# Kernel optimization log

Hardware: AMD Instinct MI355X
Metric: run time of the kernel (lower is better)

Reference implementation:

```python
import jax, jax.numpy as jnp
import numpy as np

IMAGE = 800.0
HIGH_THRESH = 0.7   # torchvision RPN fg_iou_thresh
LOW_THRESH = 0.3    # torchvision RPN bg_iou_thresh
BELOW_LOW = -1      # Matcher.BELOW_LOW_THRESHOLD
BETWEEN = -2        # Matcher.BETWEEN_THRESHOLDS


def _make_boxes(key, shape, max_wh):
    # shape = (..., 4) target; build valid xyxy boxes inside the image
    k1, k2 = jax.random.split(key)
    xy = jax.random.uniform(k1, shape[:-1] + (2,)) * (IMAGE - max_wh)
    wh = jax.random.uniform(k2, shape[:-1] + (2,)) * (max_wh - 4.0) + 4.0
    return jnp.concatenate([xy, xy + wh], axis=-1)


def setup_inputs() -> dict:
    key = jax.random.key(0)
    kA, kG, kS, kC = jax.random.split(key, 4)
    B, A, G = 4, 160000, 64
    anchors = _make_boxes(kA, (B, A, 4), 128.0)
    gt_boxes = _make_boxes(kG, (B, G, 4), 200.0)
    # soft score labels in {0, 0.5, 1} style: mostly 1, some <1 (ignored), some 0
    u = jax.random.uniform(kS, (B, G))
    score_labels = jnp.where(u < 0.15, 0.0, jnp.where(u < 0.3, 0.5, 1.0)).astype(jnp.float32)
    confidence_labels = jax.random.randint(kC, (B, G), 0, 2).astype(jnp.int32)
    return {"anchors": anchors, "gt_boxes": gt_boxes,
            "score_labels": score_labels, "confidence_labels": confidence_labels}


def _box_iou(a, b):
    # a: [G,4] gt, b: [A,4] anchors -> [G,A]
    area_a = (a[:, 2] - a[:, 0]) * (a[:, 3] - a[:, 1])          # [G]
    area_b = (b[:, 2] - b[:, 0]) * (b[:, 3] - b[:, 1])          # [A]
    lt = jnp.maximum(a[:, None, :2], b[None, :, :2])            # [G,A,2]
    rb = jnp.minimum(a[:, None, 2:], b[None, :, 2:])            # [G,A,2]
    wh = jnp.clip(rb - lt, 0.0)
    inter = wh[..., 0] * wh[..., 1]                              # [G,A]
    return inter / (area_a[:, None] + area_b[None, :] - inter)


def _matcher(mq):
    # torchvision Matcher with allow_low_quality_matches=True. mq: [G,A]
    matched_vals = mq.max(axis=0)                                # [A]
    matches = mq.argmax(axis=0).astype(jnp.int32)                # [A]
    m = jnp.where(matched_vals < LOW_THRESH, BELOW_LOW,
                  jnp.where(matched_vals < HIGH_THRESH, BETWEEN, matches))
    # restore, for each gt, anchors achieving that gt's max IoU
    highest_per_gt = mq.max(axis=1, keepdims=True)               # [G,1]
    low_quality = (mq == highest_per_gt).any(axis=0)             # [A]
    return jnp.where(low_quality, matches, m)


def _assign_one(anchors, gt, scores, confs):
    mq = _box_iou(gt, anchors)                                   # [G,A]
    midx = _matcher(mq)                                          # [A]
    cl = jnp.clip(midx, 0)
    matched_gt = gt[cl]                                          # [A,4]
    pos = midx >= 0
    labels = pos.astype(jnp.float32)
    labels = jnp.minimum(labels, scores[cl])
    labels = jnp.where(midx == BELOW_LOW, 0.0, labels)
    labels = jnp.where(midx == BETWEEN, -1.0, labels)
    labels = jnp.where((scores[cl] < 1.0) & pos, -1.0, labels)
    labels = jnp.where((confs[cl] == 0) & pos, -1.0, labels)
    return labels, matched_gt


def reference(anchors, gt_boxes, score_labels, confidence_labels):
    labels, matched_gt_boxes = jax.vmap(_assign_one)(anchors, gt_boxes, score_labels, confidence_labels)
    return labels, matched_gt_boxes
```

## Files before the change

kernel.cpp:

```cpp
#include <hip/hip_runtime.h>

constexpr int NB = 4;
constexpr int NA = 160000;
constexpr int NG = 64;

constexpr int P1   = 250;
constexpr int APB1 = NA / P1;
constexpr int APW  = 40;
constexpr int AB2  = 512;
constexpr int GX2  = (NA + AB2 - 1) / AB2;

__device__ __forceinline__ float box_area(float x0, float y0, float x1, float y1) {
#pragma clang fp contract(off)
    return (x1 - x0) * (y1 - y0);
}

__device__ __forceinline__ void inter_denom(float gx0, float gy0, float gx1, float gy1, float garea,
                                            float ax0, float ay0, float ax1, float ay1, float aarea,
                                            float& inter, float& denom) {
#pragma clang fp contract(off)
    float ltx = fmaxf(gx0, ax0);
    float lty = fmaxf(gy0, ay0);
    float rbx = fminf(gx1, ax1);
    float rby = fminf(gy1, ay1);
    float w = fmaxf(rbx - ltx, 0.0f);
    float h = fmaxf(rby - lty, 0.0f);
    inter = w * h;
    float s = garea + aarea;
    denom = s - inter;
}

__device__ __forceinline__ bool frac_gt(float i1, float d1, float i2, float d2) {
#pragma clang fp contract(off)
    float p1 = i1 * d2;
    float p2 = i2 * d1;
    float e1 = fmaf(i1, d2, -p1);
    float e2 = fmaf(i2, d1, -p2);
    return (p1 > p2) || ((p1 == p2) && (e1 > e2));
}

__device__ __forceinline__ float div_rn(float n, float d) {
    float y = __builtin_amdgcn_rcpf(d);
    float e = fmaf(-d, y, 1.0f);
    y = fmaf(e, y, y);
    float q = n * y;
    float r = fmaf(-d, q, n);
    q = fmaf(r, y, q);
    float r2 = fmaf(-d, q, n);
    return fmaf(r2, y, q);
}

__global__ __launch_bounds__(1024, 2) void k_part(
        const float* __restrict__ anchors, const float* __restrict__ gts,
        float2* __restrict__ part ) {
    __shared__ float4 sa[APB1];
    __shared__ float pi[16][NG], pd[16][NG];

    const int b = blockIdx.y;
    const int j = blockIdx.x;
    const int lane = threadIdx.x & 63;
    const int wid = __builtin_amdgcn_readfirstlane(threadIdx.x >> 6);

    const float4* __restrict__ anc =
        reinterpret_cast<const float4*>(anchors) + (size_t)b * NA;
    if (threadIdx.x < APB1)
        sa[threadIdx.x] = anc[j * APB1 + threadIdx.x];

    float4 g = reinterpret_cast<const float4*>(gts)[b * NG + lane];
    float garea = box_area(g.x, g.y, g.z, g.w);
    __syncthreads();

    float bi = 0.0f, bd = 1.0f;
#pragma unroll 8
    for (int i = 0; i < APW; ++i) {
        float4 a = sa[wid * APW + i];
        float aarea = box_area(a.x, a.y, a.z, a.w);
        float inter, denom;
        inter_denom(g.x, g.y, g.z, g.w, garea, a.x, a.y, a.z, a.w, aarea,
                    inter, denom);
        if (frac_gt(inter, denom, bi, bd)) { bi = inter; bd = denom; }
    }

    pi[wid][lane] = bi;
    pd[wid][lane] = bd;
    __syncthreads();
    if (threadIdx.x < NG) {
        float ci = pi[0][threadIdx.x], cd = pd[0][threadIdx.x];
#pragma unroll
        for (int wv = 1; wv < 16; ++wv) {
            float ni = pi[wv][threadIdx.x], nd = pd[wv][threadIdx.x];
            if (frac_gt(ni, nd, ci, cd)) { ci = ni; cd = nd; }
        }
        part[((size_t)b * P1 + j) * NG + threadIdx.x] = make_float2(ci, cd);
    }
}

__global__ __launch_bounds__(256, 2) void k_assign2(
        const float* __restrict__ anchors, const float* __restrict__ gts,
        const float* __restrict__ scores, const int* __restrict__ confs,
        const float2* __restrict__ part,
        float* __restrict__ labels_out, float4* __restrict__ boxes_out) {
    __shared__ float4 sg[NG];
    __shared__ float2 sah[NG];
    __shared__ float  ssc[NG];
    __shared__ int    scf[NG];
    __shared__ float  rpi[4][NG], rpd[4][NG];

    const int b = blockIdx.y;
    if (threadIdx.x < NG) {
        const int gi = threadIdx.x;
        sg[gi]  = reinterpret_cast<const float4*>(gts)[b * NG + gi];
        ssc[gi] = scores[b * NG + gi];
        scf[gi] = confs[b * NG + gi];
    }

    {
        const int gi = threadIdx.x & 63;
        const int c  = threadIdx.x >> 6;
        float ci = 0.0f, cd = 1.0f;
#pragma unroll 8
        for (int p = c; p < P1; p += 4) {
            float2 v = part[((size_t)b * P1 + p) * NG + gi];
            if (frac_gt(v.x, v.y, ci, cd)) { ci = v.x; cd = v.y; }
        }
        rpi[c][gi] = ci;
        rpd[c][gi] = cd;
    }
    __syncthreads();
    if (threadIdx.x < NG) {
        const int gi = threadIdx.x;
        float ci = rpi[0][gi], cd = rpd[0][gi];
#pragma unroll
        for (int wv = 1; wv < 4; ++wv) {
            float ni = rpi[wv][gi], nd = rpd[wv][gi];
            if (frac_gt(ni, nd, ci, cd)) { ci = ni; cd = nd; }
        }
        float4 gv = sg[gi];
        sah[gi] = make_float2(box_area(gv.x, gv.y, gv.z, gv.w),
                              div_rn(ci, cd));
    }
    __syncthreads();

    const int base2 = blockIdx.x * AB2;
    const float4* __restrict__ anc =
        reinterpret_cast<const float4*>(anchors) + (size_t)b * NA;

    float4 av[2];
    float  aarea[2];
    float  best[2]    = {-1.0f, -1.0f};
    int    matches[2] = {0, 0};
    bool   lowq[2]    = {false, false};
#pragma unroll
    for (int k = 0; k < 2; ++k) {
        int ai = base2 + threadIdx.x + k * 256;
        int ac = ai < NA ? ai : NA - 1;
        av[k] = anc[ac];
        aarea[k] = box_area(av[k].x, av[k].y, av[k].z, av[k].w);
    }

#pragma unroll 4
    for (int g = 0; g < NG; ++g) {
        float4 gb = sg[g];
        float2 ah = sah[g];
#pragma unroll
        for (int k = 0; k < 2; ++k) {
            float inter, denom;
            inter_denom(gb.x, gb.y, gb.z, gb.w, ah.x,
                        av[k].x, av[k].y, av[k].z, av[k].w, aarea[k],
                        inter, denom);
            float v = div_rn(inter, denom);
            if (v > best[k]) { best[k] = v; matches[k] = g; }
            lowq[k] |= (v == ah.y);
        }
    }

#pragma unroll
    for (int k = 0; k < 2; ++k) {
        int ai = base2 + threadIdx.x + k * 256;
        if (ai >= NA) continue;

        int m    = (best[k] < 0.3f) ? -1 : ((best[k] < 0.7f) ? -2 : matches[k]);
        int midx = lowq[k] ? matches[k] : m;
        int cl   = (midx < 0) ? 0 : midx;

        float4 mg = sg[cl];
        float  sc = ssc[cl];
        int    cf = scf[cl];

        bool pos = (midx >= 0);
        float lab = pos ? 1.0f : 0.0f;
        lab = fminf(lab, sc);
        if (midx == -1) lab = 0.0f;
        if (midx == -2) lab = -1.0f;
        if (sc < 1.0f && pos) lab = -1.0f;
        if (cf == 0 && pos) lab = -1.0f;

        labels_out[(size_t)b * NA + ai] = lab;
        boxes_out[(size_t)b * NA + ai] = mg;
    }
}

__global__ __launch_bounds__(256) void k_gt_highest_fb(
        const float* __restrict__ anchors, const float* __restrict__ gts,
        float* __restrict__ highest ) {
    const int b = blockIdx.y;
    const int lane = threadIdx.x & 63;
    const int wid = __builtin_amdgcn_readfirstlane(threadIdx.x >> 6);

    const float4* __restrict__ anc =
        reinterpret_cast<const float4*>(anchors) + (size_t)b * NA;
    float4 g = reinterpret_cast<const float4*>(gts)[b * NG + lane];
    float garea = box_area(g.x, g.y, g.z, g.w);

    const int base = blockIdx.x * 160 + wid * 40;
    float bi = 0.0f, bd = 1.0f;
#pragma unroll 8
    for (int i = 0; i < 40; ++i) {
        float4 a = anc[base + i];
        float aarea = box_area(a.x, a.y, a.z, a.w);
        float inter, denom;
        inter_denom(g.x, g.y, g.z, g.w, garea, a.x, a.y, a.z, a.w, aarea,
                    inter, denom);
        if (frac_gt(inter, denom, bi, bd)) { bi = inter; bd = denom; }
    }

    __shared__ float pi[4][NG], pd[4][NG];
    pi[wid][lane] = bi;
    pd[wid][lane] = bd;
    __syncthreads();
    if (threadIdx.x < NG) {
        float ci = pi[0][threadIdx.x], cd = pd[0][threadIdx.x];
#pragma unroll
        for (int wv = 1; wv < 4; ++wv) {
            float ni = pi[wv][threadIdx.x], nd = pd[wv][threadIdx.x];
            if (frac_gt(ni, nd, ci, cd)) { ci = ni; cd = nd; }
        }
        atomicMax(reinterpret_cast<int*>(&highest[b * NG + threadIdx.x]),
                  __float_as_int(div_rn(ci, cd)));
    }
}

__global__ __launch_bounds__(256) void k_assign_fb(
        const float* __restrict__ anchors, const float* __restrict__ gts,
        const float* __restrict__ scores, const int* __restrict__ confs,
        const float* __restrict__ highest,
        float* __restrict__ labels_out, float4* __restrict__ boxes_out) {
    __shared__ float4 sg[NG];
    __shared__ float2 sah[NG];
    __shared__ float  ssc[NG];
    __shared__ int    scf[NG];

    const int b = blockIdx.y;
    if (threadIdx.x < NG) {
        const int gi = threadIdx.x;
        float4 gv = reinterpret_cast<const float4*>(gts)[b * NG + gi];
        sg[gi] = gv;
        sah[gi] = make_float2(box_area(gv.x, gv.y, gv.z, gv.w),
                              highest[b * NG + gi]);
        ssc[gi] = scores[b * NG + gi];
        scf[gi] = confs[b * NG + gi];
    }
    __syncthreads();

    const int ai = blockIdx.x * 256 + threadIdx.x;
    const float4* __restrict__ anc =
        reinterpret_cast<const float4*>(anchors) + (size_t)b * NA;
    float4 av = anc[ai];
    float aarea = box_area(av.x, av.y, av.z, av.w);

    float best = -1.0f;
    int   matches = 0;
    bool  lowq = false;
#pragma unroll 4
    for (int g = 0; g < NG; ++g) {
        float4 gb = sg[g];
        float2 ah = sah[g];
        float inter, denom;
        inter_denom(gb.x, gb.y, gb.z, gb.w, ah.x,
                    av.x, av.y, av.z, av.w, aarea, inter, denom);
        float v = div_rn(inter, denom);
        if (v > best) { best = v; matches = g; }
        lowq |= (v == ah.y);
    }

    int m    = (best < 0.3f) ? -1 : ((best < 0.7f) ? -2 : matches);
    int midx = lowq ? matches : m;
    int cl   = (midx < 0) ? 0 : midx;

    float4 mg = sg[cl];
    float  sc = ssc[cl];
    int    cf = scf[cl];

    bool pos = (midx >= 0);
    float lab = pos ? 1.0f : 0.0f;
    lab = fminf(lab, sc);
    if (midx == -1) lab = 0.0f;
    if (midx == -2) lab = -1.0f;
    if (sc < 1.0f && pos) lab = -1.0f;
    if (cf == 0 && pos) lab = -1.0f;

    labels_out[(size_t)b * NA + ai] = lab;
    boxes_out[(size_t)b * NA + ai] = mg;
}

extern "C" void kernel_launch(void* const* d_in, const int* in_sizes, int n_in,
                              void* d_out, int out_size, void* d_ws, size_t ws_size,
                              hipStream_t stream) {
    const float* anchors = (const float*)d_in[0];
    const float* gts     = (const float*)d_in[1];
    const float* scores  = (const float*)d_in[2];
    const int*   confs   = (const int*)d_in[3];

    float* labels_out = (float*)d_out;
    float4* boxes_out = (float4*)((float*)d_out + (size_t)NB * NA);

    const size_t need = (size_t)NB * P1 * NG * sizeof(float2);
    if (ws_size >= need) {
        float2* part = (float2*)d_ws;
        dim3 g1(P1, NB), g2(GX2, NB);
        k_part<<<g1, dim3(1024), 0, stream>>>(anchors, gts, part);
        k_assign2<<<g2, dim3(256), 0, stream>>>(anchors, gts, scores, confs,
                                                part, labels_out, boxes_out);
    } else {
        float* highest = (float*)d_ws;
        hipMemsetAsync(d_ws, 0, (size_t)NB * NG * sizeof(float), stream);
        dim3 g1(1000, NB), g2(625, NB), blk(256);
        k_gt_highest_fb<<<g1, blk, 0, stream>>>(anchors, gts, highest);
        k_assign_fb<<<g2, blk, 0, stream>>>(anchors, gts, scores, confs,
                                            highest, labels_out, boxes_out);
    }
}
```

Measured before the change: 137.4 us.

## Fold partial-max reduction into k_part via last-block atomic counter

The first kernel now reduces its per-block partial maxima in the last-arriving block per batch, using a global atomic counter and agent-scope atomic loads and stores. It writes the final per-gt highest IoU directly. The assign kernel now reads precomputed highest values instead of re-reducing 250 partials in every block, and it processes one anchor per thread with a 625-block grid and higher occupancy launch bounds. This removes redundant per-block reduction work, at the cost of a serialized tail reduction and a counter that relies on modulo wraparound across calls.

```diff
diff --git a/kernel.cpp b/kernel.cpp
--- a/kernel.cpp
+++ b/kernel.cpp
@@ -7,8 +7,8 @@
 constexpr int P1   = 250;
 constexpr int APB1 = NA / P1;
 constexpr int APW  = 40;
-constexpr int AB2  = 512;
-constexpr int GX2  = (NA + AB2 - 1) / AB2;
+
+__device__ int g_ctr[NB];
 
 __device__ __forceinline__ float box_area(float x0, float y0, float x1, float y1) {
 #pragma clang fp contract(off)
@@ -50,11 +50,22 @@
     return fmaf(r2, y, q);
 }
 
-__global__ __launch_bounds__(1024, 2) void k_part(
+__device__ __forceinline__ unsigned long long pack2(float x, float y) {
+    return (unsigned long long)__float_as_uint(x) |
+           ((unsigned long long)__float_as_uint(y) << 32);
+}
+__device__ __forceinline__ void unpack2(unsigned long long u, float& x, float& y) {
+    x = __uint_as_float((unsigned)(u & 0xffffffffu));
+    y = __uint_as_float((unsigned)(u >> 32));
+}
+
+__global__ __launch_bounds__(1024, 8) void k_part(
         const float* __restrict__ anchors, const float* __restrict__ gts,
-        float2* __restrict__ part ) {
+        float2* __restrict__ part ,
+        float* __restrict__ highest ) {
     __shared__ float4 sa[APB1];
     __shared__ float pi[16][NG], pd[16][NG];
+    __shared__ int s_old;
 
     const int b = blockIdx.y;
     const int j = blockIdx.x;
@@ -71,7 +82,7 @@
     __syncthreads();
 
     float bi = 0.0f, bd = 1.0f;
-#pragma unroll 8
+#pragma unroll 4
     for (int i = 0; i < APW; ++i) {
         float4 a = sa[wid * APW + i];
         float aarea = box_area(a.x, a.y, a.z, a.w);
@@ -91,156 +102,49 @@
             float ni = pi[wv][threadIdx.x], nd = pd[wv][threadIdx.x];
             if (frac_gt(ni, nd, ci, cd)) { ci = ni; cd = nd; }
         }
-        part[((size_t)b * P1 + j) * NG + threadIdx.x] = make_float2(ci, cd);
-    }
-}
-
-__global__ __launch_bounds__(256, 2) void k_assign2(
-        const float* __restrict__ anchors, const float* __restrict__ gts,
-        const float* __restrict__ scores, const int* __restrict__ confs,
-        const float2* __restrict__ part,
-        float* __restrict__ labels_out, float4* __restrict__ boxes_out) {
-    __shared__ float4 sg[NG];
-    __shared__ float2 sah[NG];
-    __shared__ float  ssc[NG];
-    __shared__ int    scf[NG];
-    __shared__ float  rpi[4][NG], rpd[4][NG];
-
-    const int b = blockIdx.y;
-    if (threadIdx.x < NG) {
-        const int gi = threadIdx.x;
-        sg[gi]  = reinterpret_cast<const float4*>(gts)[b * NG + gi];
-        ssc[gi] = scores[b * NG + gi];
-        scf[gi] = confs[b * NG + gi];
-    }
+        __hip_atomic_store(
+            reinterpret_cast<unsigned long long*>(
+                &part[((size_t)b * P1 + j) * NG + threadIdx.x]),
+            pack2(ci, cd), __ATOMIC_RELAXED, __HIP_MEMORY_SCOPE_AGENT);
+    }
+    __syncthreads();
+    if (threadIdx.x == 0) {
+        __threadfence();
+        s_old = atomicAdd(&g_ctr[b], 1);
+    }
+    __syncthreads();
+    if ((s_old % P1) != P1 - 1) return;
 
     {
         const int gi = threadIdx.x & 63;
         const int c  = threadIdx.x >> 6;
         float ci = 0.0f, cd = 1.0f;
-#pragma unroll 8
-        for (int p = c; p < P1; p += 4) {
-            float2 v = part[((size_t)b * P1 + p) * NG + gi];
-            if (frac_gt(v.x, v.y, ci, cd)) { ci = v.x; cd = v.y; }
-        }
-        rpi[c][gi] = ci;
-        rpd[c][gi] = cd;
-    }
-    __syncthreads();
-    if (threadIdx.x < NG) {
-        const int gi = threadIdx.x;
-        float ci = rpi[0][gi], cd = rpd[0][gi];
-#pragma unroll
-        for (int wv = 1; wv < 4; ++wv) {
-            float ni = rpi[wv][gi], nd = rpd[wv][gi];
-            if (frac_gt(ni, nd, ci, cd)) { ci = ni; cd = nd; }
-        }
-        float4 gv = sg[gi];
-        sah[gi] = make_float2(box_area(gv.x, gv.y, gv.z, gv.w),
-                              div_rn(ci, cd));
-    }
-    __syncthreads();
-
-    const int base2 = blockIdx.x * AB2;
-    const float4* __restrict__ anc =
-        reinterpret_cast<const float4*>(anchors) + (size_t)b * NA;
-
-    float4 av[2];
-    float  aarea[2];
-    float  best[2]    = {-1.0f, -1.0f};
-    int    matches[2] = {0, 0};
-    bool   lowq[2]    = {false, false};
-#pragma unroll
-    for (int k = 0; k < 2; ++k) {
-        int ai = base2 + threadIdx.x + k * 256;
-        int ac = ai < NA ? ai : NA - 1;
-        av[k] = anc[ac];
-        aarea[k] = box_area(av[k].x, av[k].y, av[k].z, av[k].w);
-    }
-
 #pragma unroll 4
-    for (int g = 0; g < NG; ++g) {
-        float4 gb = sg[g];
-        float2 ah = sah[g];
-#pragma unroll
-        for (int k = 0; k < 2; ++k) {
-            float inter, denom;
-            inter_denom(gb.x, gb.y, gb.z, gb.w, ah.x,
-                        av[k].x, av[k].y, av[k].z, av[k].w, aarea[k],
-                        inter, denom);
-            float v = div_rn(inter, denom);
-            if (v > best[k]) { best[k] = v; matches[k] = g; }
-            lowq[k] |= (v == ah.y);
-        }
-    }
-
-#pragma unroll
-    for (int k = 0; k < 2; ++k) {
-        int ai = base2 + threadIdx.x + k * 256;
-        if (ai >= NA) continue;
-
-        int m    = (best[k] < 0.3f) ? -1 : ((best[k] < 0.7f) ? -2 : matches[k]);
-        int midx = lowq[k] ? matches[k] : m;
-        int cl   = (midx < 0) ? 0 : midx;
-
-        float4 mg = sg[cl];
-        float  sc = ssc[cl];
-        int    cf = scf[cl];
-
-        bool pos = (midx >= 0);
-        float lab = pos ? 1.0f : 0.0f;
-        lab = fminf(lab, sc);
-        if (midx == -1) lab = 0.0f;
-        if (midx == -2) lab = -1.0f;
-        if (sc < 1.0f && pos) lab = -1.0f;
-        if (cf == 0 && pos) lab = -1.0f;
-
-        labels_out[(size_t)b * NA + ai] = lab;
-        boxes_out[(size_t)b * NA + ai] = mg;
-    }
-}
-
-__global__ __launch_bounds__(256) void k_gt_highest_fb(
-        const float* __restrict__ anchors, const float* __restrict__ gts,
-        float* __restrict__ highest ) {
-    const int b = blockIdx.y;
-    const int lane = threadIdx.x & 63;
-    const int wid = __builtin_amdgcn_readfirstlane(threadIdx.x >> 6);
-
-    const float4* __restrict__ anc =
-        reinterpret_cast<const float4*>(anchors) + (size_t)b * NA;
-    float4 g = reinterpret_cast<const float4*>(gts)[b * NG + lane];
-    float garea = box_area(g.x, g.y, g.z, g.w);
-
-    const int base = blockIdx.x * 160 + wid * 40;
-    float bi = 0.0f, bd = 1.0f;
-#pragma unroll 8
-    for (int i = 0; i < 40; ++i) {
-        float4 a = anc[base + i];
-        float aarea = box_area(a.x, a.y, a.z, a.w);
-        float inter, denom;
-        inter_denom(g.x, g.y, g.z, g.w, garea, a.x, a.y, a.z, a.w, aarea,
-                    inter, denom);
-        if (frac_gt(inter, denom, bi, bd)) { bi = inter; bd = denom; }
-    }
-
-    __shared__ float pi[4][NG], pd[4][NG];
-    pi[wid][lane] = bi;
-    pd[wid][lane] = bd;
+        for (int p = c; p < P1; p += 16) {
+            unsigned long long u = __hip_atomic_load(
+                reinterpret_cast<const unsigned long long*>(
+                    &part[((size_t)b * P1 + p) * NG + gi]),
+                __ATOMIC_RELAXED, __HIP_MEMORY_SCOPE_AGENT);
+            float ni, nd;
+            unpack2(u, ni, nd);
+            if (frac_gt(ni, nd, ci, cd)) { ci = ni; cd = nd; }
+        }
+        pi[c][gi] = ci;
+        pd[c][gi] = cd;
+    }
     __syncthreads();
     if (threadIdx.x < NG) {
         float ci = pi[0][threadIdx.x], cd = pd[0][threadIdx.x];
 #pragma unroll
-        for (int wv = 1; wv < 4; ++wv) {
+        for (int wv = 1; wv < 16; ++wv) {
             float ni = pi[wv][threadIdx.x], nd = pd[wv][threadIdx.x];
             if (frac_gt(ni, nd, ci, cd)) { ci = ni; cd = nd; }
         }
-        atomicMax(reinterpret_cast<int*>(&highest[b * NG + threadIdx.x]),
-                  __float_as_int(div_rn(ci, cd)));
-    }
-}
-
-__global__ __launch_bounds__(256) void k_assign_fb(
+        highest[b * NG + threadIdx.x] = div_rn(ci, cd);
+    }
+}
+
+__global__ __launch_bounds__(256, 8) void k_assign2(
         const float* __restrict__ anchors, const float* __restrict__ gts,
         const float* __restrict__ scores, const int* __restrict__ confs,
         const float* __restrict__ highest,
@@ -254,7 +158,7 @@
     if (threadIdx.x < NG) {
         const int gi = threadIdx.x;
         float4 gv = reinterpret_cast<const float4*>(gts)[b * NG + gi];
-        sg[gi] = gv;
+        sg[gi]  = gv;
         sah[gi] = make_float2(box_area(gv.x, gv.y, gv.z, gv.w),
                               highest[b * NG + gi]);
         ssc[gi] = scores[b * NG + gi];
@@ -303,6 +207,46 @@
     boxes_out[(size_t)b * NA + ai] = mg;
 }
 
+__global__ __launch_bounds__(256) void k_gt_highest_fb(
+        const float* __restrict__ anchors, const float* __restrict__ gts,
+        float* __restrict__ highest ) {
+    const int b = blockIdx.y;
+    const int lane = threadIdx.x & 63;
+    const int wid = __builtin_amdgcn_readfirstlane(threadIdx.x >> 6);
+
+    const float4* __restrict__ anc =
+        reinterpret_cast<const float4*>(anchors) + (size_t)b * NA;
+    float4 g = reinterpret_cast<const float4*>(gts)[b * NG + lane];
+    float garea = box_area(g.x, g.y, g.z, g.w);
+
+    const int base = blockIdx.x * 160 + wid * 40;
+    float bi = 0.0f, bd = 1.0f;
+#pragma unroll 8
+    for (int i = 0; i < 40; ++i) {
+        float4 a = anc[base + i];
+        float aarea = box_area(a.x, a.y, a.z, a.w);
+        float inter, denom;
+        inter_denom(g.x, g.y, g.z, g.w, garea, a.x, a.y, a.z, a.w, aarea,
+                    inter, denom);
+        if (frac_gt(inter, denom, bi, bd)) { bi = inter; bd = denom; }
+    }
+
+    __shared__ float pi[4][NG], pd[4][NG];
+    pi[wid][lane] = bi;
+    pd[wid][lane] = bd;
+    __syncthreads();
+    if (threadIdx.x < NG) {
+        float ci = pi[0][threadIdx.x], cd = pd[0][threadIdx.x];
+#pragma unroll
+        for (int wv = 1; wv < 4; ++wv) {
+            float ni = pi[wv][threadIdx.x], nd = pd[wv][threadIdx.x];
+            if (frac_gt(ni, nd, ci, cd)) { ci = ni; cd = nd; }
+        }
+        atomicMax(reinterpret_cast<int*>(&highest[b * NG + threadIdx.x]),
+                  __float_as_int(div_rn(ci, cd)));
+    }
+}
+
 extern "C" void kernel_launch(void* const* d_in, const int* in_sizes, int n_in,
                               void* d_out, int out_size, void* d_ws, size_t ws_size,
                               hipStream_t stream) {
@@ -314,19 +258,21 @@
     float* labels_out = (float*)d_out;
     float4* boxes_out = (float4*)((float*)d_out + (size_t)NB * NA);
 
-    const size_t need = (size_t)NB * P1 * NG * sizeof(float2);
+    const size_t part_bytes = (size_t)NB * P1 * NG * sizeof(float2);
+    const size_t need = part_bytes + (size_t)NB * NG * sizeof(float);
     if (ws_size >= need) {
-        float2* part = (float2*)d_ws;
-        dim3 g1(P1, NB), g2(GX2, NB);
-        k_part<<<g1, dim3(1024), 0, stream>>>(anchors, gts, part);
+        float2* part   = (float2*)d_ws;
+        float* highest = (float*)((char*)d_ws + part_bytes);
+        dim3 g1(P1, NB), g2(625, NB);
+        k_part<<<g1, dim3(1024), 0, stream>>>(anchors, gts, part, highest);
         k_assign2<<<g2, dim3(256), 0, stream>>>(anchors, gts, scores, confs,
-                                                part, labels_out, boxes_out);
+                                                highest, labels_out, boxes_out);
     } else {
         float* highest = (float*)d_ws;
         hipMemsetAsync(d_ws, 0, (size_t)NB * NG * sizeof(float), stream);
         dim3 g1(1000, NB), g2(625, NB), blk(256);
         k_gt_highest_fb<<<g1, blk, 0, stream>>>(anchors, gts, highest);
-        k_assign_fb<<<g2, blk, 0, stream>>>(anchors, gts, scores, confs,
-                                            highest, labels_out, boxes_out);
-    }
-}
+        k_assign2<<<g2, blk, 0, stream>>>(anchors, gts, scores, confs,
+                                          highest, labels_out, boxes_out);
+    }
+}
```

Result: faster. 133.1 us (-3.1%).
